# Kernel tuning notes

Measured on AMD Instinct MI355X. Metric: run time of the kernel, lower is better.

Reference implementation:

```python
import jax, jax.numpy as jnp
import numpy as np

N_GENE, N_PATH, N_VACC = 50000, 20000, 10000
N_TOT = N_GENE + N_PATH + N_VACC
HID = 128
E_PER = 250000
K_APPNP = 8
ALPHA = 0.1
N_LAYERS = 2


def setup_inputs() -> dict:
    key = jax.random.key(0)
    ks = iter(jax.random.split(key, 40))
    f32 = jnp.float32

    def nrm(shape, scale=1.0):
        return jax.random.normal(next(ks), shape, dtype=f32) * scale

    def edges(n_src, n_dst):
        src = jax.random.randint(next(ks), (E_PER,), 0, n_src)
        dst = jax.random.randint(next(ks), (E_PER,), 0, n_dst)
        return jnp.stack([src, dst]).astype(jnp.int32)

    return {
        "x_gene": nrm((N_GENE, 256)),
        "x_pathway": nrm((N_PATH, 128)),
        "x_vaccine": nrm((N_VACC, 64)),
        "win_gene": nrm((HID, 256), 256 ** -0.5),
        "bin_gene": jnp.zeros((HID,), f32),
        "win_pathway": nrm((HID, 128), 128 ** -0.5),
        "bin_pathway": jnp.zeros((HID,), f32),
        "win_vaccine": nrm((HID, 64), 64 ** -0.5),
        "bin_vaccine": jnp.zeros((HID,), f32),
        "w_sage_l": nrm((N_LAYERS, 4, HID, HID), HID ** -0.5),
        "b_sage_l": jnp.zeros((N_LAYERS, 4, HID), f32),
        "w_sage_r": nrm((N_LAYERS, 4, HID, HID), HID ** -0.5),
        "ei_targets": edges(N_VACC, N_GENE),    # vaccine -> gene
        "ei_in": edges(N_GENE, N_PATH),         # gene -> pathway
        "ei_contains": edges(N_PATH, N_GENE),   # pathway -> gene
        "ei_interacts": edges(N_GENE, N_GENE),  # gene -> gene
    }


def _sage(x_src, x_dst, ei, wl, bl, wr, n_dst):
    # PyG SAGEConv(aggr='mean'): lin_l(mean_j x_src[j]) + lin_r(x_dst); bias lives in lin_l
    src, dst = ei[0], ei[1]
    s = jax.ops.segment_sum(x_src[src], dst, num_segments=n_dst)
    cnt = jax.ops.segment_sum(jnp.ones((ei.shape[1],), x_src.dtype), dst, num_segments=n_dst)
    agg = s / jnp.maximum(cnt, 1.0)[:, None]  # isolated dst nodes -> 0
    return agg @ wl.T + bl + x_dst @ wr.T


def _forward(x_gene, x_pathway, x_vaccine, win_gene, bin_gene, win_pathway, bin_pathway,
             win_vaccine, bin_vaccine, w_sage_l, b_sage_l, w_sage_r,
             ei_targets, ei_in, ei_contains, ei_interacts):
    # input projections + relu
    hg = jax.nn.relu(x_gene @ win_gene.T + bin_gene)
    hp = jax.nn.relu(x_pathway @ win_pathway.T + bin_pathway)
    hv = jax.nn.relu(x_vaccine @ win_vaccine.T + bin_vaccine)
    # hetero SAGE layers with residual + relu (dropout: eval mode -> identity)
    for l in range(N_LAYERS):
        o_tg = _sage(hv, hg, ei_targets, w_sage_l[l, 0], b_sage_l[l, 0], w_sage_r[l, 0], N_GENE)
        o_in = _sage(hg, hp, ei_in, w_sage_l[l, 1], b_sage_l[l, 1], w_sage_r[l, 1], N_PATH)
        o_ct = _sage(hp, hg, ei_contains, w_sage_l[l, 2], b_sage_l[l, 2], w_sage_r[l, 2], N_GENE)
        o_ii = _sage(hg, hg, ei_interacts, w_sage_l[l, 3], b_sage_l[l, 3], w_sage_r[l, 3], N_GENE)
        hg = jax.nn.relu(hg + (o_tg + o_ct + o_ii) / 3.0)  # HeteroConv aggr='mean' over 3 relations
        hp = jax.nn.relu(hp + o_in)
        hv = jax.nn.relu(hv)  # no incoming relation -> zero message
    # APPNP on homogeneous graph; node order = [gene | pathway | vaccine]
    OG, OP, OV = 0, N_GENE, N_GENE + N_PATH
    loops = jnp.arange(N_TOT, dtype=jnp.int32)
    row = jnp.concatenate([ei_targets[0] + OV, ei_in[0] + OG, ei_contains[0] + OP, ei_interacts[0] + OG, loops])
    col = jnp.concatenate([ei_targets[1] + OG, ei_in[1] + OP, ei_contains[1] + OG, ei_interacts[1] + OG, loops])
    deg = jax.ops.segment_sum(jnp.ones(row.shape, hg.dtype), col, num_segments=N_TOT)
    dinv = jnp.where(deg > 0, deg ** -0.5, 0.0)
    norm = (dinv[row] * dinv[col])[:, None]
    h0 = jnp.concatenate([hg, hp, hv], axis=0)  # [N_TOT, HID]

    def step(z, _):
        m = jax.ops.segment_sum(norm * z[row], col, num_segments=N_TOT)
        return (1.0 - ALPHA) * m + ALPHA * h0, None

    z, _ = jax.lax.scan(step, h0, None, length=K_APPNP)
    return z  # [N_TOT, HID]; rows 0:50000 gene, 50000:70000 pathway, 70000:80000 vaccine


def reference(x_gene, x_pathway, x_vaccine, win_gene, bin_gene, win_pathway, bin_pathway,
              win_vaccine, bin_vaccine, w_sage_l, b_sage_l, w_sage_r,
              ei_targets, ei_in, ei_contains, ei_interacts):
    return _forward(x_gene, x_pathway, x_vaccine, win_gene, bin_gene, win_pathway, bin_pathway,
                    win_vaccine, bin_vaccine, w_sage_l, b_sage_l, w_sage_r,
                    ei_targets, ei_in, ei_contains, ei_interacts)
```

## Files before the change

kernel.cpp:

```cpp
#include <hip/hip_runtime.h>

#define N_GENE 50000
#define N_PATH 20000
#define N_VACC 10000
#define N_TOT  80000
#define HID    128
#define E_PER  250000
#define OG 0
#define OP 50000
#define OV 70000

#define WLA_N 70000
#define NBLK_E 245

typedef _Float16  f16x8  __attribute__((ext_vector_type(8)));
typedef float     f32x4  __attribute__((ext_vector_type(4)));

__constant__ int c_segn[4] = {N_GENE, N_PATH, N_GENE, N_GENE};
__constant__ int c_soff[4] = {OV, OG, OP, OG};

struct Off4 { int* p[4]; };
struct Ei4 { const int* p[4]; };
struct AggSeg { const int* rows; const int* off; _Float16* out; int ldo; int n; };
struct Agg4 { AggSeg s[4]; };


__global__ void p1hist_kernel(Ei4 ei, int* __restrict__ bh)
{
    __shared__ int h[256];
    int t = threadIdx.x, bx = blockIdx.x, rel = blockIdx.y;
    h[t] = 0;
    __syncthreads();
    const int* dstp = ei.p[rel] + E_PER;
    int e0 = bx * 1024 + t * 4;
#pragma unroll
    for (int j = 0; j < 4; j++) {
        int e = e0 + j;
        if (e < E_PER) atomicAdd(&h[dstp[e] >> 8], 1);
    }
    __syncthreads();
    bh[((size_t)rel * NBLK_E + bx) * 256 + t] = h[t];
}

__global__ void p1scan_kernel(int* __restrict__ bh, int* __restrict__ tot)
{
    int t = threadIdx.x, hb = blockIdx.x, rel = blockIdx.y;
    int v = (t < NBLK_E) ? bh[((size_t)rel * NBLK_E + t) * 256 + hb] : 0;
    __shared__ int sh[256];
    sh[t] = v;
    __syncthreads();
    for (int d = 1; d < 256; d <<= 1) {
        int u = (t >= d) ? sh[t - d] : 0;
        __syncthreads();
        sh[t] += u;
        __syncthreads();
    }
    if (t < NBLK_E) bh[((size_t)rel * NBLK_E + t) * 256 + hb] = sh[t] - v;
    if (t == 255) tot[rel * 256 + hb] = sh[255];
}

__global__ void p1base_kernel(const int* __restrict__ tot, int* __restrict__ base)
{
    __shared__ int lt[1024];
    int t = threadIdx.x;
#pragma unroll
    for (int r = 0; r < 4; r++) lt[r * 256 + t] = tot[r * 256 + t];
    __syncthreads();
    if (t < 4) {
        int run = 0;
        for (int h = 0; h < 256; h++) { int v = lt[t * 256 + h]; lt[t * 256 + h] = run; run += v; }
    }
    __syncthreads();
#pragma unroll
    for (int r = 0; r < 4; r++) base[r * 256 + t] = lt[r * 256 + t];
}

__global__ void p1scatter_kernel(Ei4 ei, const int* __restrict__ bh, const int* __restrict__ base,
                                 unsigned long long* __restrict__ kp1)
{
    __shared__ int run[256];
    int t = threadIdx.x, bx = blockIdx.x, rel = blockIdx.y;
    run[t] = base[rel * 256 + t] + bh[((size_t)rel * NBLK_E + bx) * 256 + t];
    __syncthreads();
    const int* srcp = ei.p[rel];
    const int* dstp = srcp + E_PER;
    unsigned long long* out = kp1 + (size_t)rel * E_PER;
    int e0 = bx * 1024 + t * 4;
#pragma unroll
    for (int j = 0; j < 4; j++) {
        int e = e0 + j;
        if (e < E_PER) {
            int d = dstp[e], s = srcp[e];
            int pos = atomicAdd(&run[d >> 8], 1);
            out[pos] = ((unsigned long long)(unsigned)d << 32) | (unsigned)s;
        }
    }
}

__global__ void p2sort_kernel(const unsigned long long* __restrict__ kp1,
                              unsigned long long* __restrict__ kp0,
                              const int* __restrict__ tot, const int* __restrict__ base)
{
    int t = threadIdx.x, hb = blockIdx.x, rel = blockIdx.y;
    int start = base[rel * 256 + hb];
    int size  = tot[rel * 256 + hb];
    if (size == 0) return;
    const unsigned long long* in = kp1 + (size_t)rel * E_PER + start;
    unsigned long long* out = kp0 + (size_t)rel * E_PER;
    __shared__ int h[256];
    __shared__ int st[256];
    h[t] = 0;
    __syncthreads();
    for (int i = t; i < size; i += 256) atomicAdd(&h[(int)(in[i] >> 32) & 255], 1);
    __syncthreads();
    int v = h[t];
    for (int d = 1; d < 256; d <<= 1) {
        int u = (t >= d) ? h[t - d] : 0;
        __syncthreads();
        h[t] += u;
        __syncthreads();
    }
    st[t] = start + h[t] - v;
    __syncthreads();
    for (int i = t; i < size; i += 256) {
        unsigned long long it = in[i];
        int lb = (int)(it >> 32) & 255;
        int pos = atomicAdd(&st[lb], 1);
        out[pos] = it;
    }
}

__global__ void offbuild_kernel(const unsigned long long* __restrict__ kp0, Off4 op)
{
    int t = threadIdx.x, bx = blockIdx.x, rel = blockIdx.y;
    const unsigned long long* in = kp0 + (size_t)rel * E_PER;
    int* off = op.p[rel];
    int nd = c_segn[rel];
    int i0 = bx * 1024 + t * 4;
#pragma unroll
    for (int j = 0; j < 4; j++) {
        int i = i0 + j;
        if (i >= E_PER) continue;
        int d1 = (int)(in[i] >> 32);
        int d0 = (i == 0) ? -1 : (int)(in[i - 1] >> 32);
        for (int d = d0 + 1; d <= d1; d++) off[d] = i;
        if (i == E_PER - 1)
            for (int d = d1 + 1; d <= nd; d++) off[d] = E_PER;
    }
}

__global__ void dinv_kernel(const int* __restrict__ r0, const int* __restrict__ r1,
                            const int* __restrict__ r2, const int* __restrict__ r3,
                            float* __restrict__ dinv, int* __restrict__ offA)
{
    int i = blockIdx.x * 256 + threadIdx.x;
    if (i >= N_TOT) return;
    int deg = 1;
    if (i < N_GENE) deg += (r0[i + 1] - r0[i]) + (r2[i + 1] - r2[i]) + (r3[i + 1] - r3[i]);
    else if (i < OV) { int k = i - OP; deg += r1[k + 1] - r1[k]; }
    dinv[i] = rsqrtf((float)deg);
    if (i <= N_GENE) offA[i] = r2[i] + r3[i];
    else if (i <= OV) offA[i] = 500000 + r1[i - OP];
}

__global__ void emit_kernel(const unsigned long long* __restrict__ kp0,
                            const float* __restrict__ dinv,
                            const int* __restrict__ off2, const int* __restrict__ off3,
                            Off4 rp, int2* __restrict__ pkAll)
{
    int t = threadIdx.x, bx = blockIdx.x, rel = blockIdx.y;
    const unsigned long long* in = kp0 + (size_t)rel * E_PER;
    int* rows = rp.p[rel];
    int2* pk1 = pkAll + 500000;
    int i0 = bx * 1024 + t * 4;
#pragma unroll
    for (int j = 0; j < 4; j++) {
        int i = i0 + j;
        if (i >= E_PER) continue;
        unsigned long long it = in[i];
        int d = (int)(it >> 32);
        int g = (int)(it & 0xFFFFFFFFu) + c_soff[rel];
        rows[i] = g;
        if (rel == 0) continue;
        int2 pv = make_int2(g, __float_as_int(dinv[g]));
        if (rel == 1) pk1[i] = pv;
        else if (rel == 2) pkAll[i + off3[d]] = pv;
        else pkAll[i + off2[d + 1]] = pv;
    }
}


__global__ void agg_all_kernel(Agg4 a, const _Float16* __restrict__ Hh)
{
    int seg = blockIdx.y;
    int t = threadIdx.x;
    int node = blockIdx.x * 32 + (t >> 3);
    if (node >= a.s[seg].n) return;
    int o0 = (t & 7) * 8;
    const int* rows = a.s[seg].rows;
    int s = a.s[seg].off[node], e = a.s[seg].off[node + 1];
    float A[16] = {};
    int i = s;
    for (; i + 4 <= e; i += 4) {
        int r0 = rows[i], r1 = rows[i + 1], r2 = rows[i + 2], r3 = rows[i + 3];
        const _Float16* b0 = &Hh[(size_t)r0 * HID + o0];
        const _Float16* b1 = &Hh[(size_t)r1 * HID + o0];
        const _Float16* b2 = &Hh[(size_t)r2 * HID + o0];
        const _Float16* b3 = &Hh[(size_t)r3 * HID + o0];
        f16x8 x0a = *(const f16x8*)b0, x0b = *(const f16x8*)(b0 + 64);
        f16x8 x1a = *(const f16x8*)b1, x1b = *(const f16x8*)(b1 + 64);
        f16x8 x2a = *(const f16x8*)b2, x2b = *(const f16x8*)(b2 + 64);
        f16x8 x3a = *(const f16x8*)b3, x3b = *(const f16x8*)(b3 + 64);
#pragma unroll
        for (int j = 0; j < 8; j++) {
            A[j]     += ((float)x0a[j] + (float)x1a[j]) + ((float)x2a[j] + (float)x3a[j]);
            A[j + 8] += ((float)x0b[j] + (float)x1b[j]) + ((float)x2b[j] + (float)x3b[j]);
        }
    }
    for (; i < e; i++) {
        const _Float16* b = &Hh[(size_t)rows[i] * HID + o0];
        f16x8 xa = *(const f16x8*)b, xb = *(const f16x8*)(b + 64);
#pragma unroll
        for (int j = 0; j < 8; j++) { A[j] += (float)xa[j]; A[j + 8] += (float)xb[j]; }
    }
    float inv = (e > s) ? 1.0f / (float)(e - s) : 0.0f;
    f16x8 oa, ob;
#pragma unroll
    for (int j = 0; j < 8; j++) { oa[j] = (_Float16)(A[j] * inv); ob[j] = (_Float16)(A[j + 8] * inv); }
    _Float16* out = a.s[seg].out + (size_t)node * a.s[seg].ldo + o0;
    *(f16x8*)out = oa;
    *(f16x8*)(out + 64) = ob;
}

__global__ void base_kernel(const _Float16* __restrict__ Hh, const int* __restrict__ r0rows,
                            const int* __restrict__ r0off, const float* __restrict__ dinv,
                            _Float16* __restrict__ base, _Float16* __restrict__ z0,
                            float* __restrict__ dout)
{
    int t = threadIdx.x;
    int node = blockIdx.x * 32 + (t >> 3);
    int o0 = (t & 7) * 8;
    size_t i0 = (size_t)node * HID + o0;
    size_t i1 = i0 + 64;
    f16x8 ha = *(const f16x8*)&Hh[i0];
    f16x8 hb = *(const f16x8*)&Hh[i1];
    if (node >= OV) {
        f32x4 oa0, oa1, ob0, ob1;
#pragma unroll
        for (int j = 0; j < 4; j++) {
            oa0[j] = (float)ha[j]; oa1[j] = (float)ha[j + 4];
            ob0[j] = (float)hb[j]; ob1[j] = (float)hb[j + 4];
        }
        *(f32x4*)&dout[i0] = oa0; *(f32x4*)&dout[i0 + 4] = oa1;
        *(f32x4*)&dout[i1] = ob0; *(f32x4*)&dout[i1 + 4] = ob1;
        return;
    }
    float A[16] = {};
    if (node < N_GENE) {
        int s = r0off[node], e = r0off[node + 1];
        int i = s;
        for (; i + 4 <= e; i += 4) {
            int r0 = r0rows[i], r1 = r0rows[i + 1], r2 = r0rows[i + 2], r3 = r0rows[i + 3];
            const _Float16* b0 = &Hh[(size_t)r0 * HID + o0];
            const _Float16* b1 = &Hh[(size_t)r1 * HID + o0];
            const _Float16* b2 = &Hh[(size_t)r2 * HID + o0];
            const _Float16* b3 = &Hh[(size_t)r3 * HID + o0];
            f16x8 x0a = *(const f16x8*)b0, x0b = *(const f16x8*)(b0 + 64);
            f16x8 x1a = *(const f16x8*)b1, x1b = *(const f16x8*)(b1 + 64);
            f16x8 x2a = *(const f16x8*)b2, x2b = *(const f16x8*)(b2 + 64);
            f16x8 x3a = *(const f16x8*)b3, x3b = *(const f16x8*)(b3 + 64);
#pragma unroll
            for (int j = 0; j < 8; j++) {
                A[j]     += ((float)x0a[j] + (float)x1a[j]) + ((float)x2a[j] + (float)x3a[j]);
                A[j + 8] += ((float)x0b[j] + (float)x1b[j]) + ((float)x2b[j] + (float)x3b[j]);
            }
        }
        for (; i < e; i++) {
            const _Float16* b = &Hh[(size_t)r0rows[i] * HID + o0];
            f16x8 xa = *(const f16x8*)b, xb = *(const f16x8*)(b + 64);
#pragma unroll
            for (int j = 0; j < 8; j++) { A[j] += (float)xa[j]; A[j + 8] += (float)xb[j]; }
        }
        float sc = 0.9f * dinv[node];
#pragma unroll
        for (int j = 0; j < 16; j++) A[j] *= sc;
    }
    f16x8 ba, bb;
#pragma unroll
    for (int j = 0; j < 8; j++) {
        ba[j] = (_Float16)(0.1f * (float)ha[j] + A[j]);
        bb[j] = (_Float16)(0.1f * (float)hb[j] + A[j + 8]);
    }
    *(f16x8*)&base[i0] = ba; *(f16x8*)&base[i1] = bb;
    *(f16x8*)&z0[i0] = ha;   *(f16x8*)&z0[i1] = hb;
}

__device__ __forceinline__ void gath8(const int2* __restrict__ pk, int s, int e, int o0,
                                      const _Float16* __restrict__ zin, float (&A)[16])
{
    int i = s;
    for (; i + 4 <= e; i += 4) {
        int2 p0 = pk[i], p1 = pk[i + 1], p2 = pk[i + 2], p3 = pk[i + 3];
        const _Float16* b0 = &zin[(size_t)p0.x * HID + o0];
        const _Float16* b1 = &zin[(size_t)p1.x * HID + o0];
        const _Float16* b2 = &zin[(size_t)p2.x * HID + o0];
        const _Float16* b3 = &zin[(size_t)p3.x * HID + o0];
        f16x8 x0a = *(const f16x8*)b0, x0b = *(const f16x8*)(b0 + 64);
        f16x8 x1a = *(const f16x8*)b1, x1b = *(const f16x8*)(b1 + 64);
        f16x8 x2a = *(const f16x8*)b2, x2b = *(const f16x8*)(b2 + 64);
        f16x8 x3a = *(const f16x8*)b3, x3b = *(const f16x8*)(b3 + 64);
        float w0 = __int_as_float(p0.y), w1 = __int_as_float(p1.y);
        float w2 = __int_as_float(p2.y), w3 = __int_as_float(p3.y);
#pragma unroll
        for (int j = 0; j < 8; j++) {
            A[j]     += ((float)x0a[j] * w0 + (float)x1a[j] * w1) + ((float)x2a[j] * w2 + (float)x3a[j] * w3);
            A[j + 8] += ((float)x0b[j] * w0 + (float)x1b[j] * w1) + ((float)x2b[j] * w2 + (float)x3b[j] * w3);
        }
    }
    for (; i < e; i++) {
        int2 p = pk[i];
        const _Float16* b = &zin[(size_t)p.x * HID + o0];
        f16x8 xa = *(const f16x8*)b, xb = *(const f16x8*)(b + 64);
        float w = __int_as_float(p.y);
#pragma unroll
        for (int j = 0; j < 8; j++) { A[j] += (float)xa[j] * w; A[j + 8] += (float)xb[j] * w; }
    }
}

template<typename OT>
__launch_bounds__(256)
__global__ void appnp_kernel(const _Float16* __restrict__ zin, OT* __restrict__ zout,
                             const _Float16* __restrict__ base,
                             const int* __restrict__ offA, const int2* __restrict__ pkAll,
                             const float* __restrict__ dinv)
{
    int t = threadIdx.x;
    int c = blockIdx.x * 32 + (t >> 3);
    if (c >= WLA_N) return;
    int o0 = (t & 7) * 8;
    float A[16] = {};
    gath8(pkAll, offA[c], offA[c + 1], o0, zin, A);
    float dc = dinv[c];
    float d2 = dc * dc;
    size_t i0 = (size_t)c * HID + o0;
    size_t i1 = i0 + 64;
    f16x8 za = *(const f16x8*)&zin[i0], zb = *(const f16x8*)&zin[i1];
    f16x8 ba = *(const f16x8*)&base[i0], bb = *(const f16x8*)&base[i1];
    float ra[8], rb[8];
#pragma unroll
    for (int j = 0; j < 8; j++) {
        ra[j] = 0.9f * (dc * A[j]     + d2 * (float)za[j]) + (float)ba[j];
        rb[j] = 0.9f * (dc * A[j + 8] + d2 * (float)zb[j]) + (float)bb[j];
    }
    if constexpr (sizeof(OT) == 2) {
        f16x8 oa, ob;
#pragma unroll
        for (int j = 0; j < 8; j++) { oa[j] = (_Float16)ra[j]; ob[j] = (_Float16)rb[j]; }
        *(f16x8*)&zout[i0] = oa;
        *(f16x8*)&zout[i1] = ob;
    } else {
        f32x4 oa0, oa1, ob0, ob1;
#pragma unroll
        for (int j = 0; j < 4; j++) {
            oa0[j] = ra[j]; oa1[j] = ra[j + 4];
            ob0[j] = rb[j]; ob1[j] = rb[j + 4];
        }
        *(f32x4*)&zout[i0] = oa0; *(f32x4*)&zout[i0 + 4] = oa1;
        *(f32x4*)&zout[i1] = ob0; *(f32x4*)&zout[i1 + 4] = ob1;
    }
}


__global__ void prep_all_kernel(const float* __restrict__ wg, const float* __restrict__ wp,
                                const float* __restrict__ wv,
                                _Float16* __restrict__ obg, _Float16* __restrict__ obp, _Float16* __restrict__ obv,
                                const float* __restrict__ wsl, const float* __restrict__ bsl,
                                const float* __restrict__ wsr,
                                _Float16* __restrict__ Wg0, _Float16* __restrict__ Wg1,
                                _Float16* __restrict__ Wp0, _Float16* __restrict__ Wp1,
                                float* __restrict__ bg0, float* __restrict__ bg1,
                                float* __restrict__ bp0, float* __restrict__ bp1)
{
    int y = blockIdx.y;
    int i = blockIdx.x * 256 + threadIdx.x;
    if (y == 0) {
        if (i < 32768) obg[i] = (_Float16)wg[i];
        if (i < 16384) obp[i] = (_Float16)wp[i];
        if (i < 8192)  obv[i] = (_Float16)wv[i];
        return;
    }
    int layer = y - 1;
    const float* WL = wsl + (size_t)layer * 4 * HID * HID;
    const float* WR = wsr + (size_t)layer * 4 * HID * HID;
    _Float16* Wg = layer ? Wg1 : Wg0;
    _Float16* Wp = layer ? Wp1 : Wp0;
    float* bg = layer ? bg1 : bg0;
    float* bp = layer ? bp1 : bp0;
    if (i < 128 * 512) {
        int nr = i >> 9, k = i & 511;
        float v;
        if (k < 128)      v = WL[0 * 16384 + nr * 128 + k];
        else if (k < 256) v = WL[2 * 16384 + nr * 128 + (k - 128)];
        else if (k < 384) v = WL[3 * 16384 + nr * 128 + (k - 256)];
        else {
            int kk = k - 384;
            v = WR[0 * 16384 + nr * 128 + kk] + WR[2 * 16384 + nr * 128 + kk] + WR[3 * 16384 + nr * 128 + kk];
        }
        Wg[i] = (_Float16)v;
    }
    if (i < 128 * 256) {
        int nr = i >> 8, k = i & 255;
        float v = (k < 128) ? WL[1 * 16384 + nr * 128 + k] : WR[1 * 16384 + nr * 128 + (k - 128)];
        Wp[i] = (_Float16)v;
    }
    if (i < 128) {
        const float* BL = bsl + (size_t)layer * 4 * HID;
        bg[i] = BL[0 * 128 + i] + BL[2 * 128 + i] + BL[3 * 128 + i];
        bp[i] = BL[1 * 128 + i];
    }
}


template<int KT, int K1, bool A_F32, bool SAGE>
__launch_bounds__(256)
__global__ void tgemm_kernel(const void* __restrict__ A1_, const _Float16* __restrict__ A2,
                             const _Float16* __restrict__ W, const float* __restrict__ bias,
                             float scale, _Float16* __restrict__ Hh, int M)
{
    __shared__ _Float16 lds[128 * 40];
    int t = threadIdx.x;
    int wave = t >> 6, lane = t & 63;
    int r = lane & 15, quad = lane >> 4;
    int mbase = blockIdx.x * 128 + wave * 32;
    int mm0 = min(mbase + r, M - 1);
    int mm1 = min(mbase + 16 + r, M - 1);
    const float* Af = (const float*)A1_;
    const _Float16* Ab = (const _Float16*)A1_;

    f32x4 acc[2][8];
#pragma unroll
    for (int s = 0; s < 2; s++)
#pragma unroll
        for (int n = 0; n < 8; n++) acc[s][n] = (f32x4){0.f, 0.f, 0.f, 0.f};

    int srow = t >> 1;
    int selt = (t & 1) * 16;

#pragma unroll
    for (int k0 = 0; k0 < KT; k0 += 32) {
        __syncthreads();
        {
            const _Float16* wsrc = W + (size_t)srow * KT + k0 + selt;
            f16x8 w0 = *(const f16x8*)wsrc;
            f16x8 w1 = *(const f16x8*)(wsrc + 8);
            *(f16x8*)&lds[srow * 40 + selt] = w0;
            *(f16x8*)&lds[srow * 40 + selt + 8] = w1;
        }
        f16x8 a0, a1;
        if constexpr (A_F32) {
            const float* p0 = Af + (size_t)mm0 * KT + k0 + quad * 8;
            const float* p1 = Af + (size_t)mm1 * KT + k0 + quad * 8;
            f32x4 x0 = *(const f32x4*)p0, x1 = *(const f32x4*)(p0 + 4);
            f32x4 y0 = *(const f32x4*)p1, y1 = *(const f32x4*)(p1 + 4);
#pragma unroll
            for (int j = 0; j < 4; j++) { a0[j] = (_Float16)x0[j]; a0[j + 4] = (_Float16)x1[j]; }
#pragma unroll
            for (int j = 0; j < 4; j++) { a1[j] = (_Float16)y0[j]; a1[j + 4] = (_Float16)y1[j]; }
        } else if (k0 < K1) {
            a0 = *(const f16x8*)(Ab + (size_t)mm0 * K1 + k0 + quad * 8);
            a1 = *(const f16x8*)(Ab + (size_t)mm1 * K1 + k0 + quad * 8);
        } else {
            a0 = *(const f16x8*)(A2 + (size_t)mm0 * 128 + (k0 - K1) + quad * 8);
            a1 = *(const f16x8*)(A2 + (size_t)mm1 * 128 + (k0 - K1) + quad * 8);
        }
        __syncthreads();
#pragma unroll
        for (int nt = 0; nt < 8; nt++) {
            f16x8 b = *(const f16x8*)&lds[(nt * 16 + r) * 40 + quad * 8];
            acc[0][nt] = __builtin_amdgcn_mfma_f32_16x16x32_f16(a0, b, acc[0][nt], 0, 0, 0);
            acc[1][nt] = __builtin_amdgcn_mfma_f32_16x16x32_f16(a1, b, acc[1][nt], 0, 0, 0);
        }
    }

#pragma unroll
    for (int sub = 0; sub < 2; sub++) {
#pragma unroll
        for (int nt = 0; nt < 8; nt++) {
            int n = nt * 16 + r;
            float bv = bias[n];
#pragma unroll
            for (int i = 0; i < 4; i++) {
                int row = mbase + sub * 16 + quad * 4 + i;
                if (row >= M) continue;
                size_t idx = (size_t)row * HID + n;
                float v;
                if constexpr (SAGE) v = fmaxf((float)Hh[idx] + (acc[sub][nt][i] + bv) * scale, 0.f);
                else                v = fmaxf(acc[sub][nt][i] + bv, 0.f);
                Hh[idx] = (_Float16)v;
            }
        }
    }
}


extern "C" void kernel_launch(void* const* d_in, const int* in_sizes, int n_in,
                              void* d_out, int out_size, void* d_ws, size_t ws_size,
                              hipStream_t stream)
{
    (void)in_sizes; (void)n_in; (void)out_size; (void)ws_size;

    const float* x_gene = (const float*)d_in[0];
    const float* x_path = (const float*)d_in[1];
    const float* x_vacc = (const float*)d_in[2];
    const float* win_g  = (const float*)d_in[3];
    const float* bin_g  = (const float*)d_in[4];
    const float* win_p  = (const float*)d_in[5];
    const float* bin_p  = (const float*)d_in[6];
    const float* win_v  = (const float*)d_in[7];
    const float* bin_v  = (const float*)d_in[8];
    const float* wsl    = (const float*)d_in[9];
    const float* bsl    = (const float*)d_in[10];
    const float* wsr    = (const float*)d_in[11];
    const int* ei_tg  = (const int*)d_in[12];
    const int* ei_ing = (const int*)d_in[13];
    const int* ei_ct  = (const int*)d_in[14];
    const int* ei_ii  = (const int*)d_in[15];

    char* p = (char*)d_ws;
    auto alloc = [&](size_t b) { char* r = p; p += (b + 255) & ~((size_t)255); return r; };

    _Float16* Hh   = (_Float16*)alloc((size_t)N_TOT * HID * 2);
    _Float16* BASE = (_Float16*)alloc((size_t)OV * HID * 2);
    _Float16* Z1   = (_Float16*)alloc((size_t)OV * HID * 2);
    _Float16* Z2   = (_Float16*)alloc((size_t)OV * HID * 2);
    _Float16* AGG_G = (_Float16*)alloc((size_t)N_GENE * 384 * 2);
    _Float16* AGG_P = (_Float16*)alloc((size_t)N_PATH * 128 * 2);
    float* dinv   = (float*)alloc((size_t)N_TOT * 4);
    int* r_rows[4], *r_off[4];
    for (int r = 0; r < 4; r++) r_rows[r] = (int*)alloc((size_t)E_PER * 4);
    r_off[0] = (int*)alloc((size_t)(N_GENE + 1) * 4);
    r_off[1] = (int*)alloc((size_t)(N_PATH + 1) * 4);
    r_off[2] = (int*)alloc((size_t)(N_GENE + 1) * 4);
    r_off[3] = (int*)alloc((size_t)(N_GENE + 1) * 4);
    int* offA = (int*)alloc((size_t)(WLA_N + 1) * 4);
    int2* pkAll = (int2*)alloc((size_t)750000 * 8);
    unsigned long long* kp0 = (unsigned long long*)alloc((size_t)4 * E_PER * 8);
    unsigned long long* kp1 = (unsigned long long*)alloc((size_t)4 * E_PER * 8);
    int* bh   = (int*)alloc((size_t)4 * NBLK_E * 256 * 4);
    int* tot  = (int*)alloc((size_t)4 * 256 * 4);
    int* basebuf = (int*)alloc((size_t)4 * 256 * 4);
    _Float16* wh_g = (_Float16*)alloc((size_t)HID * 256 * 2);
    _Float16* wh_p = (_Float16*)alloc((size_t)HID * 128 * 2);
    _Float16* wh_v = (_Float16*)alloc((size_t)HID * 64 * 2);
    _Float16* Wg[2]; _Float16* Wp[2]; float* bg[2]; float* bp[2];
    for (int l = 0; l < 2; l++) {
        Wg[l] = (_Float16*)alloc((size_t)128 * 512 * 2);
        Wp[l] = (_Float16*)alloc((size_t)128 * 256 * 2);
        bg[l] = (float*)alloc(128 * 4);
        bp[l] = (float*)alloc(128 * 4);
    }

    const int TB_G = (N_GENE + 127) / 128;
    const int TB_P = (N_PATH + 127) / 128;
    const int TB_V = (N_VACC + 127) / 128;

    prep_all_kernel<<<dim3(256, 3), 256, 0, stream>>>(win_g, win_p, win_v, wh_g, wh_p, wh_v,
                                                      wsl, bsl, wsr, Wg[0], Wg[1], Wp[0], Wp[1],
                                                      bg[0], bg[1], bp[0], bp[1]);

    Ei4 e4;
    e4.p[0] = ei_tg; e4.p[1] = ei_ing; e4.p[2] = ei_ct; e4.p[3] = ei_ii;
    p1hist_kernel<<<dim3(NBLK_E, 4), 256, 0, stream>>>(e4, bh);
    p1scan_kernel<<<dim3(256, 4), 256, 0, stream>>>(bh, tot);
    p1base_kernel<<<1, 256, 0, stream>>>(tot, basebuf);
    p1scatter_kernel<<<dim3(NBLK_E, 4), 256, 0, stream>>>(e4, bh, basebuf, kp1);
    p2sort_kernel<<<dim3(256, 4), 256, 0, stream>>>(kp1, kp0, tot, basebuf);

    Off4 op;
    op.p[0] = r_off[0]; op.p[1] = r_off[1]; op.p[2] = r_off[2]; op.p[3] = r_off[3];
    offbuild_kernel<<<dim3(NBLK_E, 4), 256, 0, stream>>>(kp0, op);

    dinv_kernel<<<(N_TOT + 255) / 256, 256, 0, stream>>>(r_off[0], r_off[1], r_off[2], r_off[3], dinv, offA);

    Off4 rp;
    rp.p[0] = r_rows[0]; rp.p[1] = r_rows[1]; rp.p[2] = r_rows[2]; rp.p[3] = r_rows[3];
    emit_kernel<<<dim3(NBLK_E, 4), 256, 0, stream>>>(kp0, dinv, r_off[2], r_off[3], rp, pkAll);

    tgemm_kernel<256, 256, true, false><<<TB_G, 256, 0, stream>>>(x_gene, nullptr, wh_g, bin_g, 1.f, Hh, N_GENE);
    tgemm_kernel<128, 128, true, false><<<TB_P, 256, 0, stream>>>(x_path, nullptr, wh_p, bin_p, 1.f,
                                                                  Hh + (size_t)OP * HID, N_PATH);
    tgemm_kernel< 64,  64, true, false><<<TB_V, 256, 0, stream>>>(x_vacc, nullptr, wh_v, bin_v, 1.f,
                                                                  Hh + (size_t)OV * HID, N_VACC);

    Agg4 ag;
    ag.s[0] = {r_rows[0], r_off[0], AGG_G + 0,   384, N_GENE};
    ag.s[1] = {r_rows[2], r_off[2], AGG_G + 128, 384, N_GENE};
    ag.s[2] = {r_rows[3], r_off[3], AGG_G + 256, 384, N_GENE};
    ag.s[3] = {r_rows[1], r_off[1], AGG_P,       128, N_PATH};
    for (int l = 0; l < 2; l++) {
        agg_all_kernel<<<dim3((N_GENE + 31) / 32, 4), 256, 0, stream>>>(ag, Hh);

        tgemm_kernel<512, 384, false, true><<<TB_G, 256, 0, stream>>>(AGG_G, Hh, Wg[l], bg[l],
                                                                      1.0f / 3.0f, Hh, N_GENE);
        tgemm_kernel<256, 128, false, true><<<TB_P, 256, 0, stream>>>(AGG_P, Hh + (size_t)OP * HID, Wp[l], bp[l],
                                                                      1.0f, Hh + (size_t)OP * HID, N_PATH);
    }

    float* dout = (float*)d_out;
    base_kernel<<<N_TOT / 32, 256, 0, stream>>>(Hh, r_rows[0], r_off[0], dinv, BASE, Z1, dout);

    const int GA = (WLA_N + 31) / 32;
    appnp_kernel<<<GA, 256, 0, stream>>>(Z1, Z2, BASE, offA, pkAll, dinv);
    appnp_kernel<<<GA, 256, 0, stream>>>(Z2, Z1, BASE, offA, pkAll, dinv);
    appnp_kernel<<<GA, 256, 0, stream>>>(Z1, Z2, BASE, offA, pkAll, dinv);
    appnp_kernel<<<GA, 256, 0, stream>>>(Z2, Z1, BASE, offA, pkAll, dinv);
    appnp_kernel<<<GA, 256, 0, stream>>>(Z1, Z2, BASE, offA, pkAll, dinv);
    appnp_kernel<<<GA, 256, 0, stream>>>(Z2, Z1, BASE, offA, pkAll, dinv);
    appnp_kernel<<<GA, 256, 0, stream>>>(Z1, Z2, BASE, offA, pkAll, dinv);
    appnp_kernel<<<GA, 256, 0, stream>>>(Z2, dout, BASE, offA, pkAll, dinv);
}
```

Before: 674.1 us.

## Split feature dimension into 8 column chunks across blocks for gather kernels

The aggregation, base and APPNP gather kernels now use two threads per node covering 16 features, and blockIdx selects one of 8 feature chunks. Each launch therefore touches a 32-byte slice of the feature rows, which is meant to keep the working set per chunk small enough to stay in cache and to give more parallelism. The packed (row, dinv) edge array is replaced by a plain row-index array, with dinv looked up per edge at gather time. In exchange, the index arrays are re-read 8 times and there are extra dinv loads per edge.

Measured after the change: 1.341 ms. 1.99x slower.

```diff
diff --git a/kernel.cpp b/kernel.cpp
--- a/kernel.cpp
+++ b/kernel.cpp
@@ -12,6 +12,11 @@
 
 #define WLA_N 70000
 #define NBLK_E 245
+#define NB_G 391
+#define NB_P 157
+#define AGG_E (3*NB_G + NB_P)
+#define NBA 547
+#define NBT 625
 
 typedef _Float16  f16x8  __attribute__((ext_vector_type(8)));
 typedef float     f32x4  __attribute__((ext_vector_type(4)));
@@ -164,14 +169,12 @@
 }
 
 __global__ void emit_kernel(const unsigned long long* __restrict__ kp0,
-                            const float* __restrict__ dinv,
                             const int* __restrict__ off2, const int* __restrict__ off3,
-                            Off4 rp, int2* __restrict__ pkAll)
+                            Off4 rp, int* __restrict__ rowsA)
 {
     int t = threadIdx.x, bx = blockIdx.x, rel = blockIdx.y;
     const unsigned long long* in = kp0 + (size_t)rel * E_PER;
     int* rows = rp.p[rel];
-    int2* pk1 = pkAll + 500000;
     int i0 = bx * 1024 + t * 4;
 #pragma unroll
     for (int j = 0; j < 4; j++) {
@@ -181,192 +184,151 @@
         int d = (int)(it >> 32);
         int g = (int)(it & 0xFFFFFFFFu) + c_soff[rel];
         rows[i] = g;
-        if (rel == 0) continue;
-        int2 pv = make_int2(g, __float_as_int(dinv[g]));
-        if (rel == 1) pk1[i] = pv;
-        else if (rel == 2) pkAll[i + off3[d]] = pv;
-        else pkAll[i + off2[d + 1]] = pv;
-    }
-}
-
-
-__global__ void agg_all_kernel(Agg4 a, const _Float16* __restrict__ Hh)
-{
-    int seg = blockIdx.y;
-    int t = threadIdx.x;
-    int node = blockIdx.x * 32 + (t >> 3);
-    if (node >= a.s[seg].n) return;
-    int o0 = (t & 7) * 8;
-    const int* rows = a.s[seg].rows;
-    int s = a.s[seg].off[node], e = a.s[seg].off[node + 1];
-    float A[16] = {};
+        if (rel == 1) rowsA[500000 + i] = g;
+        else if (rel == 2) rowsA[i + off3[d]] = g;
+        else if (rel == 3) rowsA[i + off2[d + 1]] = g;
+    }
+}
+
+
+__device__ __forceinline__ void gaths(const int* __restrict__ rows, int s, int e, int o0,
+                                      const _Float16* __restrict__ src, float (&A)[8])
+{
     int i = s;
     for (; i + 4 <= e; i += 4) {
         int r0 = rows[i], r1 = rows[i + 1], r2 = rows[i + 2], r3 = rows[i + 3];
-        const _Float16* b0 = &Hh[(size_t)r0 * HID + o0];
-        const _Float16* b1 = &Hh[(size_t)r1 * HID + o0];
-        const _Float16* b2 = &Hh[(size_t)r2 * HID + o0];
-        const _Float16* b3 = &Hh[(size_t)r3 * HID + o0];
-        f16x8 x0a = *(const f16x8*)b0, x0b = *(const f16x8*)(b0 + 64);
-        f16x8 x1a = *(const f16x8*)b1, x1b = *(const f16x8*)(b1 + 64);
-        f16x8 x2a = *(const f16x8*)b2, x2b = *(const f16x8*)(b2 + 64);
-        f16x8 x3a = *(const f16x8*)b3, x3b = *(const f16x8*)(b3 + 64);
-#pragma unroll
-        for (int j = 0; j < 8; j++) {
-            A[j]     += ((float)x0a[j] + (float)x1a[j]) + ((float)x2a[j] + (float)x3a[j]);
-            A[j + 8] += ((float)x0b[j] + (float)x1b[j]) + ((float)x2b[j] + (float)x3b[j]);
-        }
+        f16x8 x0 = *(const f16x8*)&src[(size_t)r0 * HID + o0];
+        f16x8 x1 = *(const f16x8*)&src[(size_t)r1 * HID + o0];
+        f16x8 x2 = *(const f16x8*)&src[(size_t)r2 * HID + o0];
+        f16x8 x3 = *(const f16x8*)&src[(size_t)r3 * HID + o0];
+#pragma unroll
+        for (int j = 0; j < 8; j++)
+            A[j] += ((float)x0[j] + (float)x1[j]) + ((float)x2[j] + (float)x3[j]);
     }
     for (; i < e; i++) {
-        const _Float16* b = &Hh[(size_t)rows[i] * HID + o0];
-        f16x8 xa = *(const f16x8*)b, xb = *(const f16x8*)(b + 64);
-#pragma unroll
-        for (int j = 0; j < 8; j++) { A[j] += (float)xa[j]; A[j + 8] += (float)xb[j]; }
-    }
-    float inv = (e > s) ? 1.0f / (float)(e - s) : 0.0f;
-    f16x8 oa, ob;
-#pragma unroll
-    for (int j = 0; j < 8; j++) { oa[j] = (_Float16)(A[j] * inv); ob[j] = (_Float16)(A[j + 8] * inv); }
-    _Float16* out = a.s[seg].out + (size_t)node * a.s[seg].ldo + o0;
-    *(f16x8*)out = oa;
-    *(f16x8*)(out + 64) = ob;
-}
-
+        f16x8 x = *(const f16x8*)&src[(size_t)rows[i] * HID + o0];
+#pragma unroll
+        for (int j = 0; j < 8; j++) A[j] += (float)x[j];
+    }
+}
+
+__device__ __forceinline__ void gathw(const int* __restrict__ rows, const float* __restrict__ dinv,
+                                      int s, int e, int o0,
+                                      const _Float16* __restrict__ zin, float (&A)[8])
+{
+    int i = s;
+    for (; i + 4 <= e; i += 4) {
+        int r0 = rows[i], r1 = rows[i + 1], r2 = rows[i + 2], r3 = rows[i + 3];
+        f16x8 x0 = *(const f16x8*)&zin[(size_t)r0 * HID + o0];
+        f16x8 x1 = *(const f16x8*)&zin[(size_t)r1 * HID + o0];
+        f16x8 x2 = *(const f16x8*)&zin[(size_t)r2 * HID + o0];
+        f16x8 x3 = *(const f16x8*)&zin[(size_t)r3 * HID + o0];
+        float w0 = dinv[r0], w1 = dinv[r1], w2 = dinv[r2], w3 = dinv[r3];
+#pragma unroll
+        for (int j = 0; j < 8; j++)
+            A[j] += ((float)x0[j] * w0 + (float)x1[j] * w1) + ((float)x2[j] * w2 + (float)x3[j] * w3);
+    }
+    for (; i < e; i++) {
+        int r = rows[i];
+        f16x8 x = *(const f16x8*)&zin[(size_t)r * HID + o0];
+        float w = dinv[r];
+#pragma unroll
+        for (int j = 0; j < 8; j++) A[j] += (float)x[j] * w;
+    }
+}
+
+__launch_bounds__(256)
+__global__ void agg_all_kernel(Agg4 a, const _Float16* __restrict__ Hh)
+{
+    int t = threadIdx.x;
+    int chunk = blockIdx.x & 7;
+    int e = blockIdx.x >> 3;
+    int seg, sb;
+    if (e < NB_G)            { seg = 0; sb = 0; }
+    else if (e < 2 * NB_G)   { seg = 1; sb = NB_G; }
+    else if (e < 3 * NB_G)   { seg = 2; sb = 2 * NB_G; }
+    else                     { seg = 3; sb = 3 * NB_G; }
+    int node = (e - sb) * 128 + (t >> 1);
+    if (node >= a.s[seg].n) return;
+    int o0 = chunk * 16 + (t & 1) * 8;
+    int s = a.s[seg].off[node], en = a.s[seg].off[node + 1];
+    float A[8] = {};
+    gaths(a.s[seg].rows, s, en, o0, Hh, A);
+    float inv = (en > s) ? 1.0f / (float)(en - s) : 0.0f;
+    f16x8 o;
+#pragma unroll
+    for (int j = 0; j < 8; j++) o[j] = (_Float16)(A[j] * inv);
+    *(f16x8*)&a.s[seg].out[(size_t)node * a.s[seg].ldo + o0] = o;
+}
+
+__launch_bounds__(256)
 __global__ void base_kernel(const _Float16* __restrict__ Hh, const int* __restrict__ r0rows,
                             const int* __restrict__ r0off, const float* __restrict__ dinv,
                             _Float16* __restrict__ base, _Float16* __restrict__ z0,
                             float* __restrict__ dout)
 {
     int t = threadIdx.x;
-    int node = blockIdx.x * 32 + (t >> 3);
-    int o0 = (t & 7) * 8;
+    int chunk = blockIdx.x & 7;
+    int node = (blockIdx.x >> 3) * 128 + (t >> 1);
+    int o0 = chunk * 16 + (t & 1) * 8;
     size_t i0 = (size_t)node * HID + o0;
-    size_t i1 = i0 + 64;
-    f16x8 ha = *(const f16x8*)&Hh[i0];
-    f16x8 hb = *(const f16x8*)&Hh[i1];
+    f16x8 h = *(const f16x8*)&Hh[i0];
     if (node >= OV) {
-        f32x4 oa0, oa1, ob0, ob1;
-#pragma unroll
-        for (int j = 0; j < 4; j++) {
-            oa0[j] = (float)ha[j]; oa1[j] = (float)ha[j + 4];
-            ob0[j] = (float)hb[j]; ob1[j] = (float)hb[j + 4];
-        }
-        *(f32x4*)&dout[i0] = oa0; *(f32x4*)&dout[i0 + 4] = oa1;
-        *(f32x4*)&dout[i1] = ob0; *(f32x4*)&dout[i1 + 4] = ob1;
+        f32x4 o0v, o1v;
+#pragma unroll
+        for (int j = 0; j < 4; j++) { o0v[j] = (float)h[j]; o1v[j] = (float)h[j + 4]; }
+        *(f32x4*)&dout[i0] = o0v;
+        *(f32x4*)&dout[i0 + 4] = o1v;
         return;
     }
-    float A[16] = {};
+    float A[8] = {};
     if (node < N_GENE) {
-        int s = r0off[node], e = r0off[node + 1];
-        int i = s;
-        for (; i + 4 <= e; i += 4) {
-            int r0 = r0rows[i], r1 = r0rows[i + 1], r2 = r0rows[i + 2], r3 = r0rows[i + 3];
-            const _Float16* b0 = &Hh[(size_t)r0 * HID + o0];
-            const _Float16* b1 = &Hh[(size_t)r1 * HID + o0];
-            const _Float16* b2 = &Hh[(size_t)r2 * HID + o0];
-            const _Float16* b3 = &Hh[(size_t)r3 * HID + o0];
-            f16x8 x0a = *(const f16x8*)b0, x0b = *(const f16x8*)(b0 + 64);
-            f16x8 x1a = *(const f16x8*)b1, x1b = *(const f16x8*)(b1 + 64);
-            f16x8 x2a = *(const f16x8*)b2, x2b = *(const f16x8*)(b2 + 64);
-            f16x8 x3a = *(const f16x8*)b3, x3b = *(const f16x8*)(b3 + 64);
-#pragma unroll
-            for (int j = 0; j < 8; j++) {
-                A[j]     += ((float)x0a[j] + (float)x1a[j]) + ((float)x2a[j] + (float)x3a[j]);
-                A[j + 8] += ((float)x0b[j] + (float)x1b[j]) + ((float)x2b[j] + (float)x3b[j]);
-            }
-        }
-        for (; i < e; i++) {
-            const _Float16* b = &Hh[(size_t)r0rows[i] * HID + o0];
-            f16x8 xa = *(const f16x8*)b, xb = *(const f16x8*)(b + 64);
-#pragma unroll
-            for (int j = 0; j < 8; j++) { A[j] += (float)xa[j]; A[j + 8] += (float)xb[j]; }
-        }
+        gaths(r0rows, r0off[node], r0off[node + 1], o0, Hh, A);
         float sc = 0.9f * dinv[node];
 #pragma unroll
-        for (int j = 0; j < 16; j++) A[j] *= sc;
-    }
-    f16x8 ba, bb;
-#pragma unroll
-    for (int j = 0; j < 8; j++) {
-        ba[j] = (_Float16)(0.1f * (float)ha[j] + A[j]);
-        bb[j] = (_Float16)(0.1f * (float)hb[j] + A[j + 8]);
-    }
-    *(f16x8*)&base[i0] = ba; *(f16x8*)&base[i1] = bb;
-    *(f16x8*)&z0[i0] = ha;   *(f16x8*)&z0[i1] = hb;
-}
-
-__device__ __forceinline__ void gath8(const int2* __restrict__ pk, int s, int e, int o0,
-                                      const _Float16* __restrict__ zin, float (&A)[16])
-{
-    int i = s;
-    for (; i + 4 <= e; i += 4) {
-        int2 p0 = pk[i], p1 = pk[i + 1], p2 = pk[i + 2], p3 = pk[i + 3];
-        const _Float16* b0 = &zin[(size_t)p0.x * HID + o0];
-        const _Float16* b1 = &zin[(size_t)p1.x * HID + o0];
-        const _Float16* b2 = &zin[(size_t)p2.x * HID + o0];
-        const _Float16* b3 = &zin[(size_t)p3.x * HID + o0];
-        f16x8 x0a = *(const f16x8*)b0, x0b = *(const f16x8*)(b0 + 64);
-        f16x8 x1a = *(const f16x8*)b1, x1b = *(const f16x8*)(b1 + 64);
-        f16x8 x2a = *(const f16x8*)b2, x2b = *(const f16x8*)(b2 + 64);
-        f16x8 x3a = *(const f16x8*)b3, x3b = *(const f16x8*)(b3 + 64);
-        float w0 = __int_as_float(p0.y), w1 = __int_as_float(p1.y);
-        float w2 = __int_as_float(p2.y), w3 = __int_as_float(p3.y);
-#pragma unroll
-        for (int j = 0; j < 8; j++) {
-            A[j]     += ((float)x0a[j] * w0 + (float)x1a[j] * w1) + ((float)x2a[j] * w2 + (float)x3a[j] * w3);
-            A[j + 8] += ((float)x0b[j] * w0 + (float)x1b[j] * w1) + ((float)x2b[j] * w2 + (float)x3b[j] * w3);
-        }
-    }
-    for (; i < e; i++) {
-        int2 p = pk[i];
-        const _Float16* b = &zin[(size_t)p.x * HID + o0];
-        f16x8 xa = *(const f16x8*)b, xb = *(const f16x8*)(b + 64);
-        float w = __int_as_float(p.y);
-#pragma unroll
-        for (int j = 0; j < 8; j++) { A[j] += (float)xa[j] * w; A[j + 8] += (float)xb[j] * w; }
-    }
+        for (int j = 0; j < 8; j++) A[j] *= sc;
+    }
+    f16x8 bo;
+#pragma unroll
+    for (int j = 0; j < 8; j++) bo[j] = (_Float16)(0.1f * (float)h[j] + A[j]);
+    *(f16x8*)&base[i0] = bo;
+    *(f16x8*)&z0[i0] = h;
 }
 
 template<typename OT>
 __launch_bounds__(256)
 __global__ void appnp_kernel(const _Float16* __restrict__ zin, OT* __restrict__ zout,
                              const _Float16* __restrict__ base,
-                             const int* __restrict__ offA, const int2* __restrict__ pkAll,
+                             const int* __restrict__ offA, const int* __restrict__ rowsA,
                              const float* __restrict__ dinv)
 {
     int t = threadIdx.x;
-    int c = blockIdx.x * 32 + (t >> 3);
+    int chunk = blockIdx.x & 7;
+    int c = (blockIdx.x >> 3) * 128 + (t >> 1);
     if (c >= WLA_N) return;
-    int o0 = (t & 7) * 8;
-    float A[16] = {};
-    gath8(pkAll, offA[c], offA[c + 1], o0, zin, A);
+    int o0 = chunk * 16 + (t & 1) * 8;
+    float A[8] = {};
+    gathw(rowsA, dinv, offA[c], offA[c + 1], o0, zin, A);
     float dc = dinv[c];
     float d2 = dc * dc;
     size_t i0 = (size_t)c * HID + o0;
-    size_t i1 = i0 + 64;
-    f16x8 za = *(const f16x8*)&zin[i0], zb = *(const f16x8*)&zin[i1];
-    f16x8 ba = *(const f16x8*)&base[i0], bb = *(const f16x8*)&base[i1];
-    float ra[8], rb[8];
-#pragma unroll
-    for (int j = 0; j < 8; j++) {
-        ra[j] = 0.9f * (dc * A[j]     + d2 * (float)za[j]) + (float)ba[j];
-        rb[j] = 0.9f * (dc * A[j + 8] + d2 * (float)zb[j]) + (float)bb[j];
-    }
+    f16x8 zi = *(const f16x8*)&zin[i0];
+    f16x8 bs = *(const f16x8*)&base[i0];
+    float res[8];
+#pragma unroll
+    for (int j = 0; j < 8; j++)
+        res[j] = 0.9f * (dc * A[j] + d2 * (float)zi[j]) + (float)bs[j];
     if constexpr (sizeof(OT) == 2) {
-        f16x8 oa, ob;
-#pragma unroll
-        for (int j = 0; j < 8; j++) { oa[j] = (_Float16)ra[j]; ob[j] = (_Float16)rb[j]; }
-        *(f16x8*)&zout[i0] = oa;
-        *(f16x8*)&zout[i1] = ob;
+        f16x8 o;
+#pragma unroll
+        for (int j = 0; j < 8; j++) o[j] = (_Float16)res[j];
+        *(f16x8*)&zout[i0] = o;
     } else {
-        f32x4 oa0, oa1, ob0, ob1;
-#pragma unroll
-        for (int j = 0; j < 4; j++) {
-            oa0[j] = ra[j]; oa1[j] = ra[j + 4];
-            ob0[j] = rb[j]; ob1[j] = rb[j + 4];
-        }
-        *(f32x4*)&zout[i0] = oa0; *(f32x4*)&zout[i0 + 4] = oa1;
-        *(f32x4*)&zout[i1] = ob0; *(f32x4*)&zout[i1 + 4] = ob1;
+        f32x4 o0v, o1v;
+#pragma unroll
+        for (int j = 0; j < 4; j++) { o0v[j] = res[j]; o1v[j] = res[j + 4]; }
+        *(f32x4*)&zout[i0] = o0v;
+        *(f32x4*)&zout[i0 + 4] = o1v;
     }
 }
 
@@ -543,7 +505,7 @@
     r_off[2] = (int*)alloc((size_t)(N_GENE + 1) * 4);
     r_off[3] = (int*)alloc((size_t)(N_GENE + 1) * 4);
     int* offA = (int*)alloc((size_t)(WLA_N + 1) * 4);
-    int2* pkAll = (int2*)alloc((size_t)750000 * 8);
+    int* rowsA = (int*)alloc((size_t)750000 * 4);
     unsigned long long* kp0 = (unsigned long long*)alloc((size_t)4 * E_PER * 8);
     unsigned long long* kp1 = (unsigned long long*)alloc((size_t)4 * E_PER * 8);
     int* bh   = (int*)alloc((size_t)4 * NBLK_E * 256 * 4);
@@ -584,7 +546,7 @@
 
     Off4 rp;
     rp.p[0] = r_rows[0]; rp.p[1] = r_rows[1]; rp.p[2] = r_rows[2]; rp.p[3] = r_rows[3];
-    emit_kernel<<<dim3(NBLK_E, 4), 256, 0, stream>>>(kp0, dinv, r_off[2], r_off[3], rp, pkAll);
+    emit_kernel<<<dim3(NBLK_E, 4), 256, 0, stream>>>(kp0, r_off[2], r_off[3], rp, rowsA);
 
     tgemm_kernel<256, 256, true, false><<<TB_G, 256, 0, stream>>>(x_gene, nullptr, wh_g, bin_g, 1.f, Hh, N_GENE);
     tgemm_kernel<128, 128, true, false><<<TB_P, 256, 0, stream>>>(x_path, nullptr, wh_p, bin_p, 1.f,
@@ -598,7 +560,7 @@
     ag.s[2] = {r_rows[3], r_off[3], AGG_G + 256, 384, N_GENE};
     ag.s[3] = {r_rows[1], r_off[1], AGG_P,       128, N_PATH};
     for (int l = 0; l < 2; l++) {
-        agg_all_kernel<<<dim3((N_GENE + 31) / 32, 4), 256, 0, stream>>>(ag, Hh);
+        agg_all_kernel<<<AGG_E * 8, 256, 0, stream>>>(ag, Hh);
 
         tgemm_kernel<512, 384, false, true><<<TB_G, 256, 0, stream>>>(AGG_G, Hh, Wg[l], bg[l],
                                                                       1.0f / 3.0f, Hh, N_GENE);
@@ -607,15 +569,15 @@
     }
 
     float* dout = (float*)d_out;
-    base_kernel<<<N_TOT / 32, 256, 0, stream>>>(Hh, r_rows[0], r_off[0], dinv, BASE, Z1, dout);
-
-    const int GA = (WLA_N + 31) / 32;
-    appnp_kernel<<<GA, 256, 0, stream>>>(Z1, Z2, BASE, offA, pkAll, dinv);
-    appnp_kernel<<<GA, 256, 0, stream>>>(Z2, Z1, BASE, offA, pkAll, dinv);
-    appnp_kernel<<<GA, 256, 0, stream>>>(Z1, Z2, BASE, offA, pkAll, dinv);
-    appnp_kernel<<<GA, 256, 0, stream>>>(Z2, Z1, BASE, offA, pkAll, dinv);
-    appnp_kernel<<<GA, 256, 0, stream>>>(Z1, Z2, BASE, offA, pkAll, dinv);
-    appnp_kernel<<<GA, 256, 0, stream>>>(Z2, Z1, BASE, offA, pkAll, dinv);
-    appnp_kernel<<<GA, 256, 0, stream>>>(Z1, Z2, BASE, offA, pkAll, dinv);
-    appnp_kernel<<<GA, 256, 0, stream>>>(Z2, dout, BASE, offA, pkAll, dinv);
-}
+    base_kernel<<<NBT * 8, 256, 0, stream>>>(Hh, r_rows[0], r_off[0], dinv, BASE, Z1, dout);
+
+    const int GA = NBA * 8;
+    appnp_kernel<<<GA, 256, 0, stream>>>(Z1, Z2, BASE, offA, rowsA, dinv);
+    appnp_kernel<<<GA, 256, 0, stream>>>(Z2, Z1, BASE, offA, rowsA, dinv);
+    appnp_kernel<<<GA, 256, 0, stream>>>(Z1, Z2, BASE, offA, rowsA, dinv);
+    appnp_kernel<<<GA, 256, 0, stream>>>(Z2, Z1, BASE, offA, rowsA, dinv);
+    appnp_kernel<<<GA, 256, 0, stream>>>(Z1, Z2, BASE, offA, rowsA, dinv);
+    appnp_kernel<<<GA, 256, 0, stream>>>(Z2, Z1, BASE, offA, rowsA, dinv);
+    appnp_kernel<<<GA, 256, 0, stream>>>(Z1, Z2, BASE, offA, rowsA, dinv);
+    appnp_kernel<<<GA, 256, 0, stream>>>(Z2, dout, BASE, offA, rowsA, dinv);
+}
```
